# Kernel optimization log

Hardware: AMD Instinct MI355X
Metric: run time of the kernel (lower is better)

Reference implementation:

```python
import jax, jax.numpy as jnp
import numpy as np

N = 100000      # nodes
E = 1600000     # edges
F_IN = 64       # num_features
H = 64          # hidden_channels
NG = 64         # graphs in batch
ALPHA = 0.5


def _lin_init(key, fan_in, fan_out):
    kw, kb = jax.random.split(key)
    bound = 1.0 / np.sqrt(fan_in)
    w = jax.random.uniform(kw, (fan_in, fan_out), jnp.float32, -bound, bound)
    b = jax.random.uniform(kb, (fan_out,), jnp.float32, -bound, bound)
    return w, b


def setup_inputs() -> dict:
    key = jax.random.key(0)
    ks = jax.random.split(key, 12)
    x = jax.random.normal(ks[0], (N, F_IN), dtype=jnp.float32)
    edge_index = jax.random.randint(ks[1], (2, E), 0, N, dtype=jnp.int32)
    batch = jnp.sort(jax.random.randint(ks[2], (N,), 0, NG, dtype=jnp.int32))
    w1s, b1s = _lin_init(ks[3], F_IN, H)
    w1d, b1d = _lin_init(ks[4], F_IN, H)
    w2s, b2s = _lin_init(ks[5], H, H)
    w2d, b2d = _lin_init(ks[6], H, H)
    w3s, b3s = _lin_init(ks[7], H, H)
    w3d, b3d = _lin_init(ks[8], H, H)
    wl1, bl1 = _lin_init(ks[9], H, 5)
    wl2, bl2 = _lin_init(ks[10], 5, 1)
    return dict(x=x, edge_index=edge_index, batch=batch,
                w1s=w1s, b1s=b1s, w1d=w1d, b1d=b1d,
                w2s=w2s, b2s=b2s, w2d=w2d, b2d=b2d,
                w3s=w3s, b3s=b3s, w3d=w3d, b3d=b3d,
                wl1=wl1, bl1=bl1, wl2=wl2, bl2=bl2)


def _dir_gcn_conv(x, row, col, ws, bs, wd, bd):
    # directional norm: D_out^{-1/2} A D_in^{-1/2} (and same recipe for A^T)
    ones = jnp.ones((row.shape[0],), x.dtype)
    deg_out = jax.ops.segment_sum(ones, row, num_segments=N)  # row-sums of A
    deg_in = jax.ops.segment_sum(ones, col, num_segments=N)   # col-sums of A
    r_out = jnp.where(deg_out > 0, deg_out ** -0.5, 0.0)
    r_in = jnp.where(deg_in > 0, deg_in ** -0.5, 0.0)
    norm = r_out[row] * r_in[col]  # per-edge weight; identical for A and A^T norms
    msg = norm[:, None] * x[col]                       # [E, F]
    adj_x = jax.ops.segment_sum(msg, row, num_segments=N)
    msg_t = norm[:, None] * x[row]
    adj_t_x = jax.ops.segment_sum(msg_t, col, num_segments=N)
    return ALPHA * (adj_x @ ws + bs) + (1.0 - ALPHA) * (adj_t_x @ wd + bd)


def reference(x, edge_index, batch,
              w1s, b1s, w1d, b1d,
              w2s, b2s, w2d, b2d,
              w3s, b3s, w3d, b3d,
              wl1, bl1, wl2, bl2):
    row, col = edge_index[0], edge_index[1]
    h = jax.nn.relu(_dir_gcn_conv(x, row, col, w1s, b1s, w1d, b1d))
    h = jax.nn.relu(_dir_gcn_conv(h, row, col, w2s, b2s, w2d, b2d))
    h = jax.nn.relu(_dir_gcn_conv(h, row, col, w3s, b3s, w3d, b3d))
    g = jax.ops.segment_max(h, batch, num_segments=NG)  # global max pool [NG, H]
    g = jax.nn.relu(g @ wl1 + bl1)
    return g @ wl2 + bl2  # [NG, 1]
```

## Files before the change

kernel.cpp:

```cpp
#include <hip/hip_runtime.h>

#define N_NODES 100000
#define N_EDGES 1600000
#define EPAD    (N_EDGES + N_NODES)
#define HDIM    64
#define NGRAPH  64
#define BLK_NODES 8
#define ALPHA_C 0.5f
#define BETA_C  0.5f
#define BW      256
#define NB      391
#define NBLK    256
#define CHUNK   ((N_EDGES + NBLK - 1) / NBLK)

typedef _Float16 h16;
typedef _Float16 h16x4 __attribute__((ext_vector_type(4)));

__global__ __launch_bounds__(512) void bucket_count(const int* __restrict__ ei,
                                                    int* __restrict__ cntTabA,
                                                    int* __restrict__ cntTabT) {
    __shared__ int cA[NB], cT[NB];
    const int tid = threadIdx.x;
    for (int i = tid; i < NB; i += 512) { cA[i] = 0; cT[i] = 0; }
    __syncthreads();
    const int e0 = blockIdx.x * CHUNK, e1 = min(e0 + CHUNK, N_EDGES);
    for (int e = e0 + tid; e < e1; e += 512) {
        int r = ei[e];
        int c = ei[N_EDGES + e];
        atomicAdd(&cA[r >> 8], 1);
        atomicAdd(&cT[c >> 8], 1);
    }
    __syncthreads();
    for (int b = tid; b < NB; b += 512) {
        cntTabA[b * NBLK + blockIdx.x] = cA[b];
        cntTabT[b * NBLK + blockIdx.x] = cT[b];
    }
}

__global__ __launch_bounds__(256) void chunk_scan(int* __restrict__ cntTabA,
                                                  int* __restrict__ cntTabT,
                                                  int* __restrict__ tot) {
    __shared__ int s[256];
    const int b = blockIdx.x, d = blockIdx.y, tid = threadIdx.x;
    int* tab = d ? cntTabT : cntTabA;
    int v = tab[b * NBLK + tid];
    s[tid] = v;
    __syncthreads();
    for (int off = 1; off < 256; off <<= 1) {
        int t = (tid >= off) ? s[tid - off] : 0;
        __syncthreads();
        s[tid] += t;
        __syncthreads();
    }
    tab[b * NBLK + tid] = s[tid] - v;
    if (tid == 255) tot[d * 512 + b] = s[255];
}

__global__ __launch_bounds__(512) void start_scan(const int* __restrict__ tot,
                                                  int* __restrict__ bktStartA,
                                                  int* __restrict__ bktStartT) {
    __shared__ int s[512];
    const int tid = threadIdx.x;
    int v = (tid < NB) ? tot[tid] : 0;
    s[tid] = v;
    __syncthreads();
    for (int off = 1; off < 512; off <<= 1) {
        int t = (tid >= off) ? s[tid - off] : 0;
        __syncthreads();
        s[tid] += t;
        __syncthreads();
    }
    if (tid < NB) bktStartA[tid] = s[tid] - v;
    if (tid == 0) bktStartA[NB] = N_EDGES;
    __syncthreads();
    int v2 = (tid < NB) ? tot[512 + tid] : 0;
    s[tid] = v2;
    __syncthreads();
    for (int off = 1; off < 512; off <<= 1) {
        int t = (tid >= off) ? s[tid - off] : 0;
        __syncthreads();
        s[tid] += t;
        __syncthreads();
    }
    if (tid < NB) bktStartT[tid] = s[tid] - v2;
    if (tid == 0) bktStartT[NB] = N_EDGES;
}

__global__ __launch_bounds__(512) void bucketize_write(const int* __restrict__ ei,
                                                       const int* __restrict__ cntTabA,
                                                       const int* __restrict__ cntTabT,
                                                       const int* __restrict__ bktStartA,
                                                       const int* __restrict__ bktStartT,
                                                       int2* __restrict__ bktA,
                                                       int2* __restrict__ bktT) {
    __shared__ int bA[NB], bT[NB];
    const int tid = threadIdx.x;
    for (int i = tid; i < NB; i += 512) {
        bA[i] = bktStartA[i] + cntTabA[i * NBLK + blockIdx.x];
        bT[i] = bktStartT[i] + cntTabT[i * NBLK + blockIdx.x];
    }
    __syncthreads();
    const int e0 = blockIdx.x * CHUNK, e1 = min(e0 + CHUNK, N_EDGES);
    for (int e = e0 + tid; e < e1; e += 512) {
        int r = ei[e];
        int c = ei[N_EDGES + e];
        int pA = atomicAdd(&bA[r >> 8], 1);
        bktA[pA] = make_int2(r, c);
        int pT = atomicAdd(&bT[c >> 8], 1);
        bktT[pT] = make_int2(c, r);
    }
}

__global__ __launch_bounds__(256) void bucket_deg(const int* __restrict__ bktStartA,
                                                  const int* __restrict__ bktStartT,
                                                  const int2* __restrict__ bktA,
                                                  const int2* __restrict__ bktT,
                                                  int* __restrict__ deg_out,
                                                  int* __restrict__ deg_in,
                                                  float* __restrict__ r_out,
                                                  float* __restrict__ r_in,
                                                  int* __restrict__ padSum) {
    __shared__ int c[BW];
    __shared__ int red[256];
    const int b = blockIdx.x, d = blockIdx.y, tid = threadIdx.x;
    const int* bs = d ? bktStartT : bktStartA;
    const int2* bkt = d ? bktT : bktA;
    int* deg = d ? deg_in : deg_out;
    float* rr = d ? r_in : r_out;
    const int node0 = b * BW;
    c[tid] = 0;
    __syncthreads();
    const int i0 = bs[b], i1 = bs[b + 1];
    for (int i = i0 + tid; i < i1; i += 256) atomicAdd(&c[bkt[i].x - node0], 1);
    __syncthreads();
    int n = node0 + tid, dg = c[tid], pad = 0;
    if (n < N_NODES) {
        deg[n] = dg;
        rr[n] = dg > 0 ? rsqrtf((float)dg) : 0.0f;
        pad = dg + (dg & 1);
    }
    red[tid] = pad;
    __syncthreads();
    for (int off = 128; off > 0; off >>= 1) {
        if (tid < off) red[tid] += red[tid + off];
        __syncthreads();
    }
    if (tid == 0) padSum[d * 512 + b] = red[0];
}

__global__ __launch_bounds__(512) void pad_scan(const int* __restrict__ padSum,
                                                int* __restrict__ padStart) {
    __shared__ int s[512];
    const int tid = threadIdx.x;
    int v = (tid < NB) ? padSum[tid] : 0;
    s[tid] = v;
    __syncthreads();
    for (int off = 1; off < 512; off <<= 1) {
        int t = (tid >= off) ? s[tid - off] : 0;
        __syncthreads();
        s[tid] += t;
        __syncthreads();
    }
    if (tid < NB) padStart[tid] = s[tid] - v;
    __syncthreads();
    int v2 = (tid < NB) ? padSum[512 + tid] : 0;
    s[tid] = v2;
    __syncthreads();
    for (int off = 1; off < 512; off <<= 1) {
        int t = (tid >= off) ? s[tid - off] : 0;
        __syncthreads();
        s[tid] += t;
        __syncthreads();
    }
    if (tid < NB) padStart[512 + tid] = s[tid] - v2;
}

__global__ __launch_bounds__(256) void node_ptr(const int* __restrict__ padStart,
                                                const int* __restrict__ deg_out,
                                                const int* __restrict__ deg_in,
                                                int* __restrict__ rowptrP,
                                                int* __restrict__ colptrP) {
    __shared__ int s[256];
    const int b = blockIdx.x, d = blockIdx.y, tid = threadIdx.x;
    const int* deg = d ? deg_in : deg_out;
    int* ptr = d ? colptrP : rowptrP;
    int n = b * BW + tid;
    int pad = 0;
    if (n < N_NODES) { int dg = deg[n]; pad = dg + (dg & 1); }
    s[tid] = pad;
    __syncthreads();
    for (int off = 1; off < 256; off <<= 1) {
        int t = (tid >= off) ? s[tid - off] : 0;
        __syncthreads();
        s[tid] += t;
        __syncthreads();
    }
    if (n < N_NODES) ptr[n] = padStart[d * 512 + b] + s[tid] - pad;
}

__global__ __launch_bounds__(512) void bucket_scatter(
        const int* __restrict__ rowptrP, const int* __restrict__ colptrP,
        const float* __restrict__ r_out, const float* __restrict__ r_in,
        const int* __restrict__ bktStartA, const int* __restrict__ bktStartT,
        const int2* __restrict__ bktA, const int2* __restrict__ bktT,
        int2* __restrict__ recA, int2* __restrict__ recT) {
    __shared__ int cur[BW];
    __shared__ float rwt[BW];
    const int b = blockIdx.x, d = blockIdx.y, tid = threadIdx.x;
    const int* ptr = d ? colptrP : rowptrP;
    const float* rt = d ? r_in : r_out;
    const float* rs = d ? r_out : r_in;
    const int* bs = d ? bktStartT : bktStartA;
    const int2* bkt = d ? bktT : bktA;
    int2* rec = d ? recT : recA;
    const int node0 = b * BW;
    if (tid < BW) {
        int n = node0 + tid;
        cur[tid] = (n < N_NODES) ? ptr[n] : 0;
        rwt[tid] = (n < N_NODES) ? rt[n] : 0.0f;
    }
    __syncthreads();
    const int i0 = bs[b], i1 = bs[b + 1];
    for (int i = i0 + tid; i < i1; i += 512) {
        int2 e = bkt[i];
        float w = rwt[e.x - node0] * rs[e.y];
        int p = atomicAdd(&cur[e.x - node0], 1);
        rec[p] = make_int2(e.y << 7, __float_as_int(w));
    }
}

__global__ __launch_bounds__(256) void cast_kernel(const float4* __restrict__ x,
                                                   h16x4* __restrict__ xh) {
    int i = blockIdx.x * 256 + threadIdx.x;
    if (i < N_NODES * 16) {
        float4 v = x[i];
        h16x4 o;
        o.x = (h16)v.x; o.y = (h16)v.y; o.z = (h16)v.z; o.w = (h16)v.w;
        xh[i] = o;
    }
}

__device__ __forceinline__ void fma4(float4& a, float w, const float4& f) {
    a.x = fmaf(w, f.x, a.x); a.y = fmaf(w, f.y, a.y);
    a.z = fmaf(w, f.z, a.z); a.w = fmaf(w, f.w, a.w);
}

__device__ __forceinline__ void fma4h(float4& a, float w, h16x4 f) {
    a.x = fmaf(w, (float)f.x, a.x);
    a.y = fmaf(w, (float)f.y, a.y);
    a.z = fmaf(w, (float)f.z, a.z);
    a.w = fmaf(w, (float)f.w, a.w);
}

__device__ __forceinline__ float4 red_s(float4 v) {
    v.x += __shfl_xor(v.x, 16); v.y += __shfl_xor(v.y, 16);
    v.z += __shfl_xor(v.z, 16); v.w += __shfl_xor(v.w, 16);
    v.x += __shfl_xor(v.x, 32); v.y += __shfl_xor(v.y, 32);
    v.z += __shfl_xor(v.z, 32); v.w += __shfl_xor(v.w, 32);
    return v;
}

__device__ __forceinline__ h16x4 ld_h4(const char* __restrict__ p) {
    return *(const h16x4*)p;
}

__device__ __forceinline__ float4 agg_dir(const char* __restrict__ hb,
                                          const int2* __restrict__ rec,
                                          int start, int deg, int q, int s) {
    float4 a0 = {0.f,0.f,0.f,0.f}, a1 = {0.f,0.f,0.f,0.f};
    float4 a2 = {0.f,0.f,0.f,0.f}, a3 = {0.f,0.f,0.f,0.f};
    const int4* rec4 = (const int4*)(rec + start);
    const int qb = q * 8;
    int k = 0;
    for (; k + 16 <= deg; k += 16) {
        int4 p0 = rec4[(k >> 1) + s];
        int4 p1 = rec4[(k >> 1) + 4 + s];
        h16x4 f0 = ld_h4(hb + p0.x + qb);
        h16x4 f1 = ld_h4(hb + p0.z + qb);
        h16x4 f2 = ld_h4(hb + p1.x + qb);
        h16x4 f3 = ld_h4(hb + p1.z + qb);
        fma4h(a0, __int_as_float(p0.y), f0);
        fma4h(a1, __int_as_float(p0.w), f1);
        fma4h(a2, __int_as_float(p1.y), f2);
        fma4h(a3, __int_as_float(p1.w), f3);
    }
    if (k + 8 <= deg) {
        int4 p = rec4[(k >> 1) + s];
        h16x4 f0 = ld_h4(hb + p.x + qb);
        h16x4 f1 = ld_h4(hb + p.z + qb);
        fma4h(a0, __int_as_float(p.y), f0);
        fma4h(a1, __int_as_float(p.w), f1);
        k += 8;
    }
    int r = deg - k;
    if (2 * s < r) {
        int4 p = rec4[(k >> 1) + s];
        h16x4 f0 = ld_h4(hb + p.x + qb);
        fma4h(a2, __int_as_float(p.y), f0);
        if (2 * s + 1 < r) {
            h16x4 f1 = ld_h4(hb + p.z + qb);
            fma4h(a3, __int_as_float(p.w), f1);
        }
    }
    a0.x += a1.x; a0.y += a1.y; a0.z += a1.z; a0.w += a1.w;
    a2.x += a3.x; a2.y += a3.y; a2.z += a3.z; a2.w += a3.w;
    a0.x += a2.x; a0.y += a2.y; a0.z += a2.z; a0.w += a2.w;
    return red_s(a0);
}

__global__ __launch_bounds__(512, 8) void layer_kernel(
        const h16* __restrict__ h_in, h16* __restrict__ h_out,
        const int* __restrict__ rowptrP, const int* __restrict__ deg_out,
        const int2* __restrict__ recA,
        const int* __restrict__ colptrP, const int* __restrict__ deg_in,
        const int2* __restrict__ recT,
        const float* __restrict__ ws, const float* __restrict__ bs,
        const float* __restrict__ wd, const float* __restrict__ bd) {
    __shared__ float4 s_ws[HDIM * 16];
    __shared__ float4 s_wd[HDIM * 16];
    __shared__ float4 s_accv[BLK_NODES][2][16];

    const int tid  = threadIdx.x;
    const int wave = tid >> 6;
    const int lane = tid & 63;
    const int q = lane & 15;
    const int s = lane >> 4;
    const int node = blockIdx.x * BLK_NODES + wave;

    const float4* wsv = (const float4*)ws;
    const float4* wdv = (const float4*)wd;
    s_ws[tid] = wsv[tid]; s_ws[tid + 512] = wsv[tid + 512];
    s_wd[tid] = wdv[tid]; s_wd[tid + 512] = wdv[tid + 512];

    const char* hb = (const char*)h_in;
    float4 aA = agg_dir(hb, recA, rowptrP[node], deg_out[node], q, s);
    if (s == 0) s_accv[wave][0][q] = aA;
    float4 aT = agg_dir(hb, recT, colptrP[node], deg_in[node], q, s);
    if (s == 0) s_accv[wave][1][q] = aT;

    __syncthreads();

    const float* accA = (const float*)&s_accv[wave][0][0];
    const float* accT = (const float*)&s_accv[wave][1][0];
    float4 oA = {0.f,0.f,0.f,0.f}, oT = {0.f,0.f,0.f,0.f};
    const int k0 = s * 16;
#pragma unroll
    for (int i = 0; i < 16; i++) {
        int k = k0 + i;
        float vA = accA[k];
        float vT = accT[k];
        float4 wA = s_ws[k * 16 + q];
        float4 wT = s_wd[k * 16 + q];
        fma4(oA, vA, wA);
        fma4(oT, vT, wT);
    }
    float4 o;
    o.x = ALPHA_C * oA.x + BETA_C * oT.x;
    o.y = ALPHA_C * oA.y + BETA_C * oT.y;
    o.z = ALPHA_C * oA.z + BETA_C * oT.z;
    o.w = ALPHA_C * oA.w + BETA_C * oT.w;
    o = red_s(o);
    if (s == 0) {
        float4 bA = ((const float4*)bs)[q];
        float4 bD = ((const float4*)bd)[q];
        o.x = fmaxf(o.x + ALPHA_C * bA.x + BETA_C * bD.x, 0.0f);
        o.y = fmaxf(o.y + ALPHA_C * bA.y + BETA_C * bD.y, 0.0f);
        o.z = fmaxf(o.z + ALPHA_C * bA.z + BETA_C * bD.z, 0.0f);
        o.w = fmaxf(o.w + ALPHA_C * bA.w + BETA_C * bD.w, 0.0f);
        h16x4 st;
        st.x = (h16)o.x; st.y = (h16)o.y; st.z = (h16)o.z; st.w = (h16)o.w;
        *(h16x4*)(h_out + (size_t)node * 64 + q * 4) = st;
    }
}

__global__ __launch_bounds__(256) void pool_kernel(const h16* __restrict__ h,
                                                   const int* __restrict__ batch,
                                                   unsigned* __restrict__ g) {
    int t = blockIdx.x * 256 + threadIdx.x;
    const int ngroups = N_NODES / 16;
    if (t >= ngroups * 64) return;
    int f = t & 63;
    int n0 = (t >> 6) * 16;
    int curg = batch[n0];
    float m = 0.0f;
    for (int n = n0; n < n0 + 16; n++) {
        int b = batch[n];
        if (b != curg) {
            atomicMax(&g[curg * HDIM + f], __float_as_uint(m));
            curg = b;
            m = 0.0f;
        }
        m = fmaxf(m, (float)h[(size_t)n * HDIM + f]);
    }
    atomicMax(&g[curg * HDIM + f], __float_as_uint(m));
}

__global__ __launch_bounds__(64) void mlp_kernel(const unsigned* __restrict__ g,
                                                 const float* __restrict__ wl1,
                                                 const float* __restrict__ bl1,
                                                 const float* __restrict__ wl2,
                                                 const float* __restrict__ bl2,
                                                 float* __restrict__ out) {
    int t = threadIdx.x;
    float gv[HDIM];
#pragma unroll
    for (int k = 0; k < HDIM; k++) gv[k] = __uint_as_float(g[t * HDIM + k]);
    float o = bl2[0];
#pragma unroll
    for (int j = 0; j < 5; j++) {
        float hj = bl1[j];
#pragma unroll
        for (int k = 0; k < HDIM; k++) hj += gv[k] * wl1[k * 5 + j];
        hj = fmaxf(hj, 0.0f);
        o += hj * wl2[j];
    }
    out[t] = o;
}

extern "C" void kernel_launch(void* const* d_in, const int* in_sizes, int n_in,
                              void* d_out, int out_size, void* d_ws, size_t ws_size,
                              hipStream_t stream) {
    const float* x   = (const float*)d_in[0];
    const int*   ei  = (const int*)d_in[1];
    const int*   bat = (const int*)d_in[2];
    const float* w1s = (const float*)d_in[3];
    const float* b1s = (const float*)d_in[4];
    const float* w1d = (const float*)d_in[5];
    const float* b1d = (const float*)d_in[6];
    const float* w2s = (const float*)d_in[7];
    const float* b2s = (const float*)d_in[8];
    const float* w2d = (const float*)d_in[9];
    const float* b2d = (const float*)d_in[10];
    const float* w3s = (const float*)d_in[11];
    const float* b3s = (const float*)d_in[12];
    const float* w3d = (const float*)d_in[13];
    const float* b3d = (const float*)d_in[14];
    const float* wl1 = (const float*)d_in[15];
    const float* bl1 = (const float*)d_in[16];
    const float* wl2 = (const float*)d_in[17];
    const float* bl2 = (const float*)d_in[18];
    float* out = (float*)d_out;

    char* p = (char*)d_ws;
    int*   deg_out = (int*)p;              p += N_NODES * 4;
    int*   deg_in  = (int*)p;              p += N_NODES * 4;
    int*   rowptrP = (int*)p;              p += N_NODES * 4;
    int*   colptrP = (int*)p;              p += N_NODES * 4;
    float* r_out   = (float*)p;            p += N_NODES * 4;
    float* r_in    = (float*)p;            p += N_NODES * 4;
    int*   cntTabA = (int*)p;              p += (size_t)NB * NBLK * 4;
    int*   cntTabT = (int*)p;              p += (size_t)NB * NBLK * 4;
    int*   totTab  = (int*)p;              p += 1024 * 4;
    int*   bktStartA = (int*)p;            p += 512 * 4;
    int*   bktStartT = (int*)p;            p += 512 * 4;
    int*   padSum  = (int*)p;              p += 1024 * 4;
    int*   padStart = (int*)p;             p += 1024 * 4;
    int2*  recA    = (int2*)p;             p += (size_t)EPAD * 8;
    int2*  recT    = (int2*)p;             p += (size_t)EPAD * 8;
    int2*  bktA    = (int2*)p;
    h16*   hA      = (h16*)p;
    int2*  bktT    = (int2*)((char*)bktA + (size_t)N_EDGES * 8);
    p = (char*)bktA + 2 * (size_t)N_EDGES * 8;
    h16*   hB      = (h16*)p;              p += (size_t)N_NODES * HDIM * 2;
    h16*   xh      = (h16*)p;              p += (size_t)N_NODES * HDIM * 2;
    unsigned* g    = (unsigned*)p;         p += NGRAPH * HDIM * 4;

    hipMemsetAsync(g, 0, NGRAPH * HDIM * 4, stream);

    cast_kernel<<<(N_NODES * 16 + 255) / 256, 256, 0, stream>>>(
        (const float4*)x, (h16x4*)xh);

    bucket_count<<<NBLK, 512, 0, stream>>>(ei, cntTabA, cntTabT);
    dim3 gb2(NB, 2);
    chunk_scan<<<gb2, 256, 0, stream>>>(cntTabA, cntTabT, totTab);
    start_scan<<<1, 512, 0, stream>>>(totTab, bktStartA, bktStartT);
    bucketize_write<<<NBLK, 512, 0, stream>>>(ei, cntTabA, cntTabT,
                                              bktStartA, bktStartT, bktA, bktT);

    dim3 gb(NB, 2);
    bucket_deg<<<gb, 256, 0, stream>>>(bktStartA, bktStartT, bktA, bktT,
                                       deg_out, deg_in, r_out, r_in, padSum);
    pad_scan<<<1, 512, 0, stream>>>(padSum, padStart);
    node_ptr<<<gb, 256, 0, stream>>>(padStart, deg_out, deg_in, rowptrP, colptrP);
    bucket_scatter<<<gb, 512, 0, stream>>>(
        rowptrP, colptrP, r_out, r_in, bktStartA, bktStartT, bktA, bktT, recA, recT);

    layer_kernel<<<N_NODES / BLK_NODES, 512, 0, stream>>>(
        xh, hA, rowptrP, deg_out, recA, colptrP, deg_in, recT, w1s, b1s, w1d, b1d);
    layer_kernel<<<N_NODES / BLK_NODES, 512, 0, stream>>>(
        hA, hB, rowptrP, deg_out, recA, colptrP, deg_in, recT, w2s, b2s, w2d, b2d);
    layer_kernel<<<N_NODES / BLK_NODES, 512, 0, stream>>>(
        hB, hA, rowptrP, deg_out, recA, colptrP, deg_in, recT, w3s, b3s, w3d, b3d);

    const int pool_threads = (N_NODES / 16) * 64;
    pool_kernel<<<(pool_threads + 255) / 256, 256, 0, stream>>>(hA, bat, g);

    mlp_kernel<<<1, 64, 0, stream>>>(g, wl1, bl1, wl2, bl2, out);
}
```

Baseline: 526.8 us.

## Split each layer into gather-aggregate kernel and MFMA fp16 dense transform

Each fused layer kernel becomes two kernels. An aggregation kernel writes both directional sums as fp16 into a 256-byte row. A separate GEMM kernel then applies the combined, pre-scaled, transposed weights with MFMA 16x16x32 fp16 instructions and writes the ReLU output in place. This removes the per-block weight staging into shared memory, the __syncthreads and the scalar FMA transform from the gather kernel, which should raise its occupancy. The cost is an extra launch plus an extra write and read of the intermediate per layer, a doubled row stride for the gathered features, and fp16 rounding of the aggregates before the matmul.

After: 504.8 us. 4.2% less time.

```diff
diff --git a/kernel.cpp b/kernel.cpp
--- a/kernel.cpp
+++ b/kernel.cpp
@@ -6,15 +6,16 @@
 #define HDIM    64
 #define NGRAPH  64
 #define BLK_NODES 8
-#define ALPHA_C 0.5f
-#define BETA_C  0.5f
 #define BW      256
 #define NB      391
 #define NBLK    256
 #define CHUNK   ((N_EDGES + NBLK - 1) / NBLK)
+#define MTILES  (N_NODES / 16)
 
 typedef _Float16 h16;
 typedef _Float16 h16x4 __attribute__((ext_vector_type(4)));
+typedef _Float16 h16x8 __attribute__((ext_vector_type(8)));
+typedef float    f32x4 __attribute__((ext_vector_type(4)));
 
 __global__ __launch_bounds__(512) void bucket_count(const int* __restrict__ ei,
                                                     int* __restrict__ cntTabA,
@@ -240,9 +241,28 @@
     }
 }
 
-__device__ __forceinline__ void fma4(float4& a, float w, const float4& f) {
-    a.x = fmaf(w, f.x, a.x); a.y = fmaf(w, f.y, a.y);
-    a.z = fmaf(w, f.z, a.z); a.w = fmaf(w, f.w, a.w);
+__global__ __launch_bounds__(256) void wprep_kernel(
+        const float* __restrict__ w1s, const float* __restrict__ w1d,
+        const float* __restrict__ w2s, const float* __restrict__ w2d,
+        const float* __restrict__ w3s, const float* __restrict__ w3d,
+        const float* __restrict__ b1s, const float* __restrict__ b1d,
+        const float* __restrict__ b2s, const float* __restrict__ b2d,
+        const float* __restrict__ b3s, const float* __restrict__ b3d,
+        h16* __restrict__ WT, float* __restrict__ bc) {
+    const int l = blockIdx.y;
+    const float* ws = l == 0 ? w1s : l == 1 ? w2s : w3s;
+    const float* wd = l == 0 ? w1d : l == 1 ? w2d : w3d;
+    int e = blockIdx.x * 256 + threadIdx.x;
+    if (e < 8192) {
+        int f = e >> 7, k = e & 127;
+        float v = (k < 64) ? ws[k * 64 + f] : wd[(k - 64) * 64 + f];
+        WT[l * 8192 + f * 128 + k] = (h16)(0.5f * v);
+    }
+    if (blockIdx.x == 0 && threadIdx.x < 64) {
+        const float* bs = l == 0 ? b1s : l == 1 ? b2s : b3s;
+        const float* bd = l == 0 ? b1d : l == 1 ? b2d : b3d;
+        bc[l * 64 + threadIdx.x] = 0.5f * (bs[threadIdx.x] + bd[threadIdx.x]);
+    }
 }
 
 __device__ __forceinline__ void fma4h(float4& a, float w, h16x4 f) {
@@ -266,7 +286,7 @@
 
 __device__ __forceinline__ float4 agg_dir(const char* __restrict__ hb,
                                           const int2* __restrict__ rec,
-                                          int start, int deg, int q, int s) {
+                                          int start, int deg, int q, int s, int sh) {
     float4 a0 = {0.f,0.f,0.f,0.f}, a1 = {0.f,0.f,0.f,0.f};
     float4 a2 = {0.f,0.f,0.f,0.f}, a3 = {0.f,0.f,0.f,0.f};
     const int4* rec4 = (const int4*)(rec + start);
@@ -275,10 +295,10 @@
     for (; k + 16 <= deg; k += 16) {
         int4 p0 = rec4[(k >> 1) + s];
         int4 p1 = rec4[(k >> 1) + 4 + s];
-        h16x4 f0 = ld_h4(hb + p0.x + qb);
-        h16x4 f1 = ld_h4(hb + p0.z + qb);
-        h16x4 f2 = ld_h4(hb + p1.x + qb);
-        h16x4 f3 = ld_h4(hb + p1.z + qb);
+        h16x4 f0 = ld_h4(hb + (p0.x << sh) + qb);
+        h16x4 f1 = ld_h4(hb + (p0.z << sh) + qb);
+        h16x4 f2 = ld_h4(hb + (p1.x << sh) + qb);
+        h16x4 f3 = ld_h4(hb + (p1.z << sh) + qb);
         fma4h(a0, __int_as_float(p0.y), f0);
         fma4h(a1, __int_as_float(p0.w), f1);
         fma4h(a2, __int_as_float(p1.y), f2);
@@ -286,8 +306,8 @@
     }
     if (k + 8 <= deg) {
         int4 p = rec4[(k >> 1) + s];
-        h16x4 f0 = ld_h4(hb + p.x + qb);
-        h16x4 f1 = ld_h4(hb + p.z + qb);
+        h16x4 f0 = ld_h4(hb + (p.x << sh) + qb);
+        h16x4 f1 = ld_h4(hb + (p.z << sh) + qb);
         fma4h(a0, __int_as_float(p.y), f0);
         fma4h(a1, __int_as_float(p.w), f1);
         k += 8;
@@ -295,10 +315,10 @@
     int r = deg - k;
     if (2 * s < r) {
         int4 p = rec4[(k >> 1) + s];
-        h16x4 f0 = ld_h4(hb + p.x + qb);
+        h16x4 f0 = ld_h4(hb + (p.x << sh) + qb);
         fma4h(a2, __int_as_float(p.y), f0);
         if (2 * s + 1 < r) {
-            h16x4 f1 = ld_h4(hb + p.z + qb);
+            h16x4 f1 = ld_h4(hb + (p.z << sh) + qb);
             fma4h(a3, __int_as_float(p.w), f1);
         }
     }
@@ -308,18 +328,12 @@
     return red_s(a0);
 }
 
-__global__ __launch_bounds__(512, 8) void layer_kernel(
-        const h16* __restrict__ h_in, h16* __restrict__ h_out,
+__global__ __launch_bounds__(512) void agg_kernel(
+        const char* __restrict__ h_in, char* __restrict__ acc_out, int sh,
         const int* __restrict__ rowptrP, const int* __restrict__ deg_out,
         const int2* __restrict__ recA,
         const int* __restrict__ colptrP, const int* __restrict__ deg_in,
-        const int2* __restrict__ recT,
-        const float* __restrict__ ws, const float* __restrict__ bs,
-        const float* __restrict__ wd, const float* __restrict__ bd) {
-    __shared__ float4 s_ws[HDIM * 16];
-    __shared__ float4 s_wd[HDIM * 16];
-    __shared__ float4 s_accv[BLK_NODES][2][16];
-
+        const int2* __restrict__ recT) {
     const int tid  = threadIdx.x;
     const int wave = tid >> 6;
     const int lane = tid & 63;
@@ -327,49 +341,54 @@
     const int s = lane >> 4;
     const int node = blockIdx.x * BLK_NODES + wave;
 
-    const float4* wsv = (const float4*)ws;
-    const float4* wdv = (const float4*)wd;
-    s_ws[tid] = wsv[tid]; s_ws[tid + 512] = wsv[tid + 512];
-    s_wd[tid] = wdv[tid]; s_wd[tid + 512] = wdv[tid + 512];
-
-    const char* hb = (const char*)h_in;
-    float4 aA = agg_dir(hb, recA, rowptrP[node], deg_out[node], q, s);
-    if (s == 0) s_accv[wave][0][q] = aA;
-    float4 aT = agg_dir(hb, recT, colptrP[node], deg_in[node], q, s);
-    if (s == 0) s_accv[wave][1][q] = aT;
-
-    __syncthreads();
-
-    const float* accA = (const float*)&s_accv[wave][0][0];
-    const float* accT = (const float*)&s_accv[wave][1][0];
-    float4 oA = {0.f,0.f,0.f,0.f}, oT = {0.f,0.f,0.f,0.f};
-    const int k0 = s * 16;
-#pragma unroll
-    for (int i = 0; i < 16; i++) {
-        int k = k0 + i;
-        float vA = accA[k];
-        float vT = accT[k];
-        float4 wA = s_ws[k * 16 + q];
-        float4 wT = s_wd[k * 16 + q];
-        fma4(oA, vA, wA);
-        fma4(oT, vT, wT);
-    }
-    float4 o;
-    o.x = ALPHA_C * oA.x + BETA_C * oT.x;
-    o.y = ALPHA_C * oA.y + BETA_C * oT.y;
-    o.z = ALPHA_C * oA.z + BETA_C * oT.z;
-    o.w = ALPHA_C * oA.w + BETA_C * oT.w;
-    o = red_s(o);
+    float4 aA = agg_dir(h_in, recA, rowptrP[node], deg_out[node], q, s, sh);
+    float4 aT = agg_dir(h_in, recT, colptrP[node], deg_in[node], q, s, sh);
     if (s == 0) {
-        float4 bA = ((const float4*)bs)[q];
-        float4 bD = ((const float4*)bd)[q];
-        o.x = fmaxf(o.x + ALPHA_C * bA.x + BETA_C * bD.x, 0.0f);
-        o.y = fmaxf(o.y + ALPHA_C * bA.y + BETA_C * bD.y, 0.0f);
-        o.z = fmaxf(o.z + ALPHA_C * bA.z + BETA_C * bD.z, 0.0f);
-        o.w = fmaxf(o.w + ALPHA_C * bA.w + BETA_C * bD.w, 0.0f);
-        h16x4 st;
-        st.x = (h16)o.x; st.y = (h16)o.y; st.z = (h16)o.z; st.w = (h16)o.w;
-        *(h16x4*)(h_out + (size_t)node * 64 + q * 4) = st;
+        h16x4 pA, pT;
+        pA.x = (h16)aA.x; pA.y = (h16)aA.y; pA.z = (h16)aA.z; pA.w = (h16)aA.w;
+        pT.x = (h16)aT.x; pT.y = (h16)aT.y; pT.z = (h16)aT.z; pT.w = (h16)aT.w;
+        char* row = acc_out + (size_t)node * 256;
+        *(h16x4*)(row + q * 8) = pA;
+        *(h16x4*)(row + 128 + q * 8) = pT;
+    }
+}
+
+__global__ __launch_bounds__(256) void gemm_kernel(char* __restrict__ acc,
+                                                   const h16* __restrict__ WT,
+                                                   const float* __restrict__ bc) {
+    const int lane = threadIdx.x & 63;
+    const int wid = (blockIdx.x * 256 + threadIdx.x) >> 6;
+    const int nW = gridDim.x * 4;
+    const int m = lane & 15, t = lane >> 4;
+
+    h16x8 bfrag[4][4];
+    float bb[4];
+#pragma unroll
+    for (int nt = 0; nt < 4; nt++) {
+        bb[nt] = bc[nt * 16 + m];
+#pragma unroll
+        for (int kk = 0; kk < 4; kk++)
+            bfrag[nt][kk] = *(const h16x8*)(WT + (nt * 16 + m) * 128 + kk * 32 + t * 8);
+    }
+
+    for (int tile = wid; tile < MTILES; tile += nW) {
+        char* arow = acc + (size_t)tile * 16 * 256;
+        h16x8 afrag[4];
+#pragma unroll
+        for (int kk = 0; kk < 4; kk++)
+            afrag[kk] = *(const h16x8*)(arow + m * 256 + kk * 64 + t * 16);
+#pragma unroll
+        for (int nt = 0; nt < 4; nt++) {
+            f32x4 c = {0.f, 0.f, 0.f, 0.f};
+#pragma unroll
+            for (int kk = 0; kk < 4; kk++)
+                c = __builtin_amdgcn_mfma_f32_16x16x32_f16(afrag[kk], bfrag[nt][kk], c, 0, 0, 0);
+#pragma unroll
+            for (int r = 0; r < 4; r++) {
+                float o = fmaxf(c[r] + bb[nt], 0.0f);
+                *(h16*)(arow + (t * 4 + r) * 256 + (nt * 16 + m) * 2) = (h16)o;
+            }
+        }
     }
 }
 
@@ -390,7 +409,7 @@
             curg = b;
             m = 0.0f;
         }
-        m = fmaxf(m, (float)h[(size_t)n * HDIM + f]);
+        m = fmaxf(m, (float)h[(size_t)n * 128 + f]);
     }
     atomicMax(&g[curg * HDIM + f], __float_as_uint(m));
 }
@@ -457,18 +476,24 @@
     int*   padStart = (int*)p;             p += 1024 * 4;
     int2*  recA    = (int2*)p;             p += (size_t)EPAD * 8;
     int2*  recT    = (int2*)p;             p += (size_t)EPAD * 8;
+    char*  bufP    = p;
     int2*  bktA    = (int2*)p;
-    h16*   hA      = (h16*)p;
-    int2*  bktT    = (int2*)((char*)bktA + (size_t)N_EDGES * 8);
-    p = (char*)bktA + 2 * (size_t)N_EDGES * 8;
-    h16*   hB      = (h16*)p;              p += (size_t)N_NODES * HDIM * 2;
-    h16*   xh      = (h16*)p;              p += (size_t)N_NODES * HDIM * 2;
+    int2*  bktT    = (int2*)(p + (size_t)N_EDGES * 8);
+    p += 2 * (size_t)N_EDGES * 8;
+    char*  bufQ    = p;
+    h16*   xh      = (h16*)p;
+    p += 2 * (size_t)N_EDGES * 8;
     unsigned* g    = (unsigned*)p;         p += NGRAPH * HDIM * 4;
+    h16*   WT      = (h16*)p;              p += 3 * 8192 * 2;
+    float* bc      = (float*)p;            p += 3 * 64 * 4;
 
     hipMemsetAsync(g, 0, NGRAPH * HDIM * 4, stream);
 
     cast_kernel<<<(N_NODES * 16 + 255) / 256, 256, 0, stream>>>(
         (const float4*)x, (h16x4*)xh);
+    dim3 gw(32, 3);
+    wprep_kernel<<<gw, 256, 0, stream>>>(w1s, w1d, w2s, w2d, w3s, w3d,
+                                         b1s, b1d, b2s, b2d, b3s, b3d, WT, bc);
 
     bucket_count<<<NBLK, 512, 0, stream>>>(ei, cntTabA, cntTabT);
     dim3 gb2(NB, 2);
@@ -485,15 +510,19 @@
     bucket_scatter<<<gb, 512, 0, stream>>>(
         rowptrP, colptrP, r_out, r_in, bktStartA, bktStartT, bktA, bktT, recA, recT);
 
-    layer_kernel<<<N_NODES / BLK_NODES, 512, 0, stream>>>(
-        xh, hA, rowptrP, deg_out, recA, colptrP, deg_in, recT, w1s, b1s, w1d, b1d);
-    layer_kernel<<<N_NODES / BLK_NODES, 512, 0, stream>>>(
-        hA, hB, rowptrP, deg_out, recA, colptrP, deg_in, recT, w2s, b2s, w2d, b2d);
-    layer_kernel<<<N_NODES / BLK_NODES, 512, 0, stream>>>(
-        hB, hA, rowptrP, deg_out, recA, colptrP, deg_in, recT, w3s, b3s, w3d, b3d);
+    const int agrid = N_NODES / BLK_NODES;
+    agg_kernel<<<agrid, 512, 0, stream>>>((const char*)xh, bufP, 0,
+                                          rowptrP, deg_out, recA, colptrP, deg_in, recT);
+    gemm_kernel<<<256, 256, 0, stream>>>(bufP, WT, bc);
+    agg_kernel<<<agrid, 512, 0, stream>>>(bufP, bufQ, 1,
+                                          rowptrP, deg_out, recA, colptrP, deg_in, recT);
+    gemm_kernel<<<256, 256, 0, stream>>>(bufQ, WT + 8192, bc + 64);
+    agg_kernel<<<agrid, 512, 0, stream>>>(bufQ, bufP, 1,
+                                          rowptrP, deg_out, recA, colptrP, deg_in, recT);
+    gemm_kernel<<<256, 256, 0, stream>>>(bufP, WT + 16384, bc + 128);
 
     const int pool_threads = (N_NODES / 16) * 64;
-    pool_kernel<<<(pool_threads + 255) / 256, 256, 0, stream>>>(hA, bat, g);
+    pool_kernel<<<(pool_threads + 255) / 256, 256, 0, stream>>>((const h16*)bufP, bat, g);
 
     mlp_kernel<<<1, 64, 0, stream>>>(g, wl1, bl1, wl2, bl2, out);
 }
```
